# Kernel optimization log

Hardware: AMD Instinct MI355X
Metric: run time of the kernel (lower is better)

The kernel has to match this reference:

```python
import jax, jax.numpy as jnp
import numpy as np

D_MODEL = 1024
N_HEAD = 16
D_K = D_MODEL // N_HEAD
B, S = 4, 2048


def setup_inputs() -> dict:
    key = jax.random.key(0)
    ks = jax.random.split(key, 12)
    def w(k):
        return jax.random.normal(k, (D_MODEL, D_MODEL), dtype=jnp.float32) * 0.02
    def b(k):
        return jax.random.normal(k, (D_MODEL,), dtype=jnp.float32) * 0.02
    return {
        "x": jax.random.normal(ks[0], (B, S, D_MODEL), dtype=jnp.float32),
        "pos_emb": jax.random.normal(ks[1], (S, D_MODEL), dtype=jnp.float32),
        "Wq": w(ks[2]), "bq": b(ks[3]),
        "Wk": w(ks[4]), "bk": b(ks[5]),
        "Wv": w(ks[6]), "bv": b(ks[7]),
        "Wp": w(ks[8]), "bp": b(ks[9]),
        "Wo": w(ks[10]), "bo": b(ks[11]),
    }


def reference(x, pos_emb, Wq, bq, Wk, bk, Wv, bv, Wp, bp, Wo, bo):
    # x: [B, S, D]; pos_emb: [S, D]. cache=None path (prefill): kv_len == S.
    Bsz, Sl, _ = x.shape
    def heads(t):  # [B, S, D] -> [B, H, S, dk]
        return t.reshape(Bsz, Sl, N_HEAD, D_K).transpose(0, 2, 1, 3)
    q = heads(x @ Wq.T + bq)
    k = heads(x @ Wk.T + bk)
    v = heads(x @ Wv.T + bv)
    # pos projection: [S, D] -> [H, S, dk]
    p = (pos_emb @ Wp.T + bp).reshape(Sl, N_HEAD, D_K).transpose(1, 0, 2)
    q_pos = q + p[None]  # broadcast over batch
    scores = jnp.einsum("bhqd,bhkd->bhqk", q_pos, k) / jnp.sqrt(jnp.asarray(D_K, x.dtype))
    # causal mask: triu(ones(S, S), diagonal=1) positions are masked
    causal = jnp.tril(jnp.ones((Sl, Sl), dtype=bool))  # True = keep
    scores = jnp.where(causal[None, None], scores, -jnp.inf)
    attn = jax.nn.softmax(scores, axis=-1)  # dropout is identity (eval / p=0)
    out = jnp.einsum("bhqk,bhkd->bhqd", attn, v)
    out = out.transpose(0, 2, 1, 3).reshape(Bsz, Sl, D_MODEL)
    return out @ Wo.T + bo
```

## Files before the change

### kernel.cpp

```cpp
#include <hip/hip_runtime.h>

#define D_MODEL 1024
#define N_HEADS 16
#define DK 64
#define BATCH 4
#define SEQ 2048
#define MROWS (BATCH * SEQ)
#define TILE_E (256 * 64)

typedef float f32x4 __attribute__((ext_vector_type(4)));
typedef short bf16x8 __attribute__((ext_vector_type(8)));
typedef unsigned short u16;
typedef unsigned short u16x8 __attribute__((ext_vector_type(8)));

__device__ __forceinline__ float bf2f(u16 u) {
    union { unsigned int i; float f; } v; v.i = ((unsigned int)u) << 16; return v.f;
}
__device__ __forceinline__ u16 f2bf(float f) {
    union { float f; unsigned int i; } v; v.f = f;
    unsigned int u = v.i;
    u += 0x7fffu + ((u >> 16) & 1u);
    return (u16)(u >> 16);
}
__device__ __forceinline__ unsigned int pk2(float a, float b) {
    union { float f; unsigned int i; } ua, ub; ua.f = a; ub.f = b;
    return __builtin_amdgcn_perm(ub.i + 0x8000u, ua.i + 0x8000u, 0x07060302u);
}
__device__ __forceinline__ unsigned int cvtpk(float a, float b) {
    unsigned int r;
    asm("v_cvt_pk_bf16_f32 %0, %1, %2" : "=v"(r) : "v"(a), "v"(b));
    return r;
}

typedef unsigned int u32_as1 __attribute__((address_space(1)));
typedef unsigned int u32_as3 __attribute__((address_space(3)));
__device__ __forceinline__ void gload16(const u16* g, u16* l) {
    __builtin_amdgcn_global_load_lds((const u32_as1*)g, (u32_as3*)l, 16, 0, 0);
}

__global__ __launch_bounds__(256) void convert_all(
    const float* __restrict__ x, const float* __restrict__ pe,
    const float* __restrict__ w0, const float* __restrict__ w1, const float* __restrict__ w2,
    const float* __restrict__ w3, const float* __restrict__ w4,
    u16* __restrict__ xb, u16* __restrict__ pb,
    u16* __restrict__ wb0, u16* __restrict__ wb1, u16* __restrict__ wb2,
    u16* __restrict__ wb3, u16* __restrict__ wb4)
{
    int t = blockIdx.x * 256 + threadIdx.x;
    const float* src; u16* dst; int idx;
    if (t < 1048576)      { src = x;  dst = xb; idx = t; }
    else if (t < 1310720) { src = pe; dst = pb; idx = t - 1048576; }
    else {
        int r = t - 1310720; int w = r >> 17; idx = r & 131071;
        if      (w == 0) { src = w0; dst = wb0; }
        else if (w == 1) { src = w1; dst = wb1; }
        else if (w == 2) { src = w2; dst = wb2; }
        else if (w == 3) { src = w3; dst = wb3; }
        else             { src = w4; dst = wb4; }
    }
    const float4* p = (const float4*)src + (size_t)idx * 2;
    float4 a = p[0], b = p[1];
    u16x8 o;
    o[0] = f2bf(a.x); o[1] = f2bf(a.y); o[2] = f2bf(a.z); o[3] = f2bf(a.w);
    o[4] = f2bf(b.x); o[5] = f2bf(b.y); o[6] = f2bf(b.z); o[7] = f2bf(b.w);
    *((u16x8*)dst + idx) = o;
}

#define SA(bufp, h, kk) do { \
    gload16(Ag + (size_t)((h) * 64) * 1024 + (kk),       (bufp) + ((h) * 64 + wv * 8) * 64); \
    gload16(Ag + (size_t)((h) * 64 + 128) * 1024 + (kk), (bufp) + ((h) * 64 + 128 + wv * 8) * 64); \
} while (0)
#define SB(bufp, h, kk) do { \
    gload16(Wg + (size_t)((h) * 32) * 1024 + (kk),       (bufp) + (wq2 * 64 + (h) * 32 + w3 * 8) * 64); \
    gload16(Wg + (size_t)((h) * 32 + 128) * 1024 + (kk), (bufp) + (128 + wq2 * 64 + (h) * 32 + w3 * 8) * 64); \
} while (0)
#define LOAD_A(mh) \
    _Pragma("unroll") \
    for (int mi = 0; mi < 4; ++mi) { \
        aA[mi][0] = *(const bf16x8*)&Abuf[aoff0 + ((mh) * 64 + mi * 16) * 64]; \
        aA[mi][1] = *(const bf16x8*)&Abuf[aoff1 + ((mh) * 64 + mi * 16) * 64]; \
    }
#define LOAD_B(nh) \
    _Pragma("unroll") \
    for (int ni = 0; ni < 2; ++ni) { \
        bB[nh][ni][0] = *(const bf16x8*)&Bbuf[boff0 + ((nh) * 32 + ni * 16) * 64]; \
        bB[nh][ni][1] = *(const bf16x8*)&Bbuf[boff1 + ((nh) * 32 + ni * 16) * 64]; \
    }
#define MFMA16(mh, nh) \
    _Pragma("unroll") \
    for (int ks = 0; ks < 2; ++ks) \
        _Pragma("unroll") \
        for (int mi = 0; mi < 4; ++mi) \
            _Pragma("unroll") \
            for (int ni = 0; ni < 2; ++ni) \
                acc[(mh) * 4 + mi][(nh) * 2 + ni] = __builtin_amdgcn_mfma_f32_16x16x32_bf16( \
                    aA[mi][ks], bB[nh][ni][ks], acc[(mh) * 4 + mi][(nh) * 2 + ni], 0, 0, 0);

__device__ __forceinline__ void gemm256_loop(
    const u16* __restrict__ Ag, const u16* __restrict__ Wg,
    u16* AsBase, u16* BsBase, int wv,
    int aoff0, int aoff1, int boff0, int boff1, f32x4 (&acc)[8][4])
{
    const int wq2 = wv >> 2, w3 = wv & 3;
    bf16x8 aA[4][2], bB[2][2][2];

    SA(AsBase, 0, 0); SB(BsBase, 0, 0); SB(BsBase, 1, 0); SA(AsBase, 1, 0);
    SA(AsBase + TILE_E, 0, 64); SB(BsBase + TILE_E, 0, 64); SA(AsBase + TILE_E, 1, 64);
    asm volatile("s_waitcnt vmcnt(6)" ::: "memory");
    __builtin_amdgcn_s_barrier();

    for (int T = 0; T < 16; ++T) {
        u16* Abuf = AsBase + (T & 1) * TILE_E;
        u16* Bbuf = BsBase + (T & 1) * TILE_E;
        u16* Both = BsBase + ((T & 1) ^ 1) * TILE_E;
        const int k2 = T * 64 + 128;

        LOAD_A(0); LOAD_B(0);
        if (T < 15) SB(Both, 1, T * 64 + 64);
        __builtin_amdgcn_s_barrier();
        asm volatile("s_waitcnt lgkmcnt(0)" ::: "memory");
        __builtin_amdgcn_s_setprio(1); MFMA16(0, 0); __builtin_amdgcn_s_setprio(0);
        __builtin_amdgcn_s_barrier();

        LOAD_B(1);
        if (T < 14) SA(Abuf, 0, k2);
        __builtin_amdgcn_s_barrier();
        asm volatile("s_waitcnt lgkmcnt(0)" ::: "memory");
        __builtin_amdgcn_s_setprio(1); MFMA16(0, 1); __builtin_amdgcn_s_setprio(0);
        __builtin_amdgcn_s_barrier();

        LOAD_A(1);
        if (T < 14) SB(Bbuf, 0, k2);
        __builtin_amdgcn_s_barrier();
        asm volatile("s_waitcnt lgkmcnt(0)" ::: "memory");
        __builtin_amdgcn_s_setprio(1); MFMA16(1, 0); __builtin_amdgcn_s_setprio(0);
        __builtin_amdgcn_s_barrier();

        if (T < 14) SA(Abuf, 1, k2);
        __builtin_amdgcn_s_barrier();
        __builtin_amdgcn_s_setprio(1); MFMA16(1, 1); __builtin_amdgcn_s_setprio(0);
        if (T < 14)      { asm volatile("s_waitcnt vmcnt(6)" ::: "memory"); }
        else if (T < 15) { asm volatile("s_waitcnt vmcnt(0)" ::: "memory"); }
        __builtin_amdgcn_s_barrier();
    }
}

__global__ __launch_bounds__(512, 2) void qkv_gemm256(
    const u16* __restrict__ xb, const u16* __restrict__ peb,
    const u16* __restrict__ wqb, const u16* __restrict__ wkb,
    const u16* __restrict__ wvb, const u16* __restrict__ wpb,
    const float* __restrict__ bq, const float* __restrict__ bk,
    const float* __restrict__ bv, const float* __restrict__ bp,
    u16* __restrict__ Qb, u16* __restrict__ Kb, u16* __restrict__ V3,
    u16* __restrict__ Pb)
{
    __shared__ __align__(16) u16 SH[4 * TILE_E];
    u16* As = SH;
    u16* Bs = SH + 2 * TILE_E;

    const int tid  = threadIdx.x;
    const int lane = tid & 63;
    const int wv   = tid >> 6;
    const int l15  = lane & 15;
    const int quad = lane >> 4;
    const int wm = wv >> 2, wn = wv & 3;

    int wg = (blockIdx.x & 7) * 52 + (blockIdx.x >> 3);
    int chunk, m0, n0;
    if (wg < 384) {
        int g = wg >> 5;
        chunk = g >> 2; n0 = (g & 3) * 256; m0 = (wg & 31) * 256;
    } else {
        int r = wg - 384;
        chunk = 3; n0 = (r >> 3) * 256; m0 = (r & 7) * 256;
    }

    const u16* Abase = (chunk == 3) ? peb : xb;
    const u16* Wbase = (chunk == 0) ? wqb : ((chunk == 1) ? wkb : ((chunk == 2) ? wvb : wpb));

    const int trow = tid >> 3;
    const int swz  = ((tid & 7) ^ (trow & 7)) * 8;
    const u16* Ag = Abase + (size_t)(m0 + trow) * 1024 + swz;
    const u16* Wg = Wbase + (size_t)(n0 + (wv >> 2) * 64 + (trow & 31)) * 1024 + swz;

    const int x7 = l15 & 7;
    const int aoff0 = (wm * 128 + l15) * 64 + ((quad    ) ^ x7) * 8;
    const int aoff1 = (wm * 128 + l15) * 64 + ((quad + 4) ^ x7) * 8;
    const int boff0 = (wn * 64 + l15) * 64 + ((quad    ) ^ x7) * 8;
    const int boff1 = (wn * 64 + l15) * 64 + ((quad + 4) ^ x7) * 8;

    f32x4 acc[8][4];
#pragma unroll
    for (int i = 0; i < 8; ++i)
#pragma unroll
        for (int j = 0; j < 4; ++j) acc[i][j] = f32x4{0.f, 0.f, 0.f, 0.f};

    gemm256_loop(Ag, Wg, As, Bs, wv, aoff0, aoff1, boff0, boff1, acc);

    const float* bias = (chunk == 0) ? bq : ((chunk == 1) ? bk : ((chunk == 2) ? bv : bp));
    const int r0 = quad * 4;
    if (chunk == 2) {
#pragma unroll
        for (int n = 0; n < 4; ++n) {
            int col = n0 + wn * 64 + n * 16 + l15;
            float bvv = bias[col];
#pragma unroll
            for (int m = 0; m < 8; ++m) {
                int row0 = m0 + wm * 128 + m * 16 + r0;
                int hh = col >> 6, d = col & 63;
                int bb = row0 >> 11, sl = row0 & 2047;
                union { u16 h[4]; uint2 v; } pk;
#pragma unroll
                for (int r = 0; r < 4; ++r) pk.h[r] = f2bf(acc[m][n][r] + bvv);
                *((uint2*)V3 + ((size_t)(bb * 16 + hh) * 512 + (sl >> 2)) * 64 + d) = pk.v;
            }
        }
    } else {
        u16* dst = (chunk == 0) ? Qb : ((chunk == 1) ? Kb : Pb);
#pragma unroll
        for (int p = 0; p < 2; ++p) {
            __syncthreads();
            if (wm == p) {
#pragma unroll
                for (int n = 0; n < 4; ++n) {
                    int colL = wn * 64 + n * 16 + l15;
                    float bvv = bias[n0 + colL];
#pragma unroll
                    for (int m = 0; m < 8; ++m) {
#pragma unroll
                        for (int r = 0; r < 4; ++r)
                            SH[(m * 16 + r0 + r) * 264 + colL] = f2bf(acc[m][n][r] + bvv);
                    }
                }
            }
            __syncthreads();
            const int rbase = m0 + p * 128;
#pragma unroll
            for (int s = 0; s < 2; ++s) {
                int rowL = (tid >> 3) + s * 64;
#pragma unroll
                for (int i = 0; i < 4; ++i) {
                    int cc = (tid & 7) + i * 8;
                    *(u16x8*)(dst + (size_t)(rbase + rowL) * 1024 + n0 + cc * 8) =
                        *(const u16x8*)&SH[rowL * 264 + cc * 8];
                }
            }
        }
    }
}

#undef SA
#undef SB
#undef LOAD_A
#undef LOAD_B
#undef MFMA16

#define A_TILE (256 * 64)
#define B_TILE (128 * 64)
#define SAo(bufp, h, kk) do { \
    gload16(Ag + (size_t)((h) * 32) * 1024 + (kk),     (bufp) + (adst + (h) * 32) * 64); \
    gload16(Ag + (size_t)((h) * 32 + 8) * 1024 + (kk), (bufp) + (adst + (h) * 32 + 8) * 64); \
} while (0)
#define SBo(bufp, nh, kk) \
    gload16(Wg + (size_t)((nh) * 32) * 1024 + (kk), (bufp) + (bdst + (nh) * 32) * 64)
#define LAo(mh) \
    _Pragma("unroll") \
    for (int mi = 0; mi < 2; ++mi) { \
        aA[mi][0] = *(const bf16x8*)&Abuf[aoff0 + ((mh) * 32 + mi * 16) * 64]; \
        aA[mi][1] = *(const bf16x8*)&Abuf[aoff1 + ((mh) * 32 + mi * 16) * 64]; \
    }
#define LBo(nh) \
    _Pragma("unroll") \
    for (int ni = 0; ni < 2; ++ni) { \
        bB[nh][ni][0] = *(const bf16x8*)&Bbuf[boff0 + ((nh) * 32 + ni * 16) * 64]; \
        bB[nh][ni][1] = *(const bf16x8*)&Bbuf[boff1 + ((nh) * 32 + ni * 16) * 64]; \
    }
#define MMo(mh, nh) \
    _Pragma("unroll") \
    for (int ks = 0; ks < 2; ++ks) \
        _Pragma("unroll") \
        for (int mi = 0; mi < 2; ++mi) \
            _Pragma("unroll") \
            for (int ni = 0; ni < 2; ++ni) \
                acc[(mh) * 2 + mi][(nh) * 2 + ni] = __builtin_amdgcn_mfma_f32_16x16x32_bf16( \
                    aA[mi][ks], bB[nh][ni][ks], acc[(mh) * 2 + mi][(nh) * 2 + ni], 0, 0, 0);

__global__ __launch_bounds__(512, 2) void gemm_out256n(
    const u16* __restrict__ A, const u16* __restrict__ W,
    const float* __restrict__ bias, float* __restrict__ Cout)
{
    __shared__ __align__(16) u16 As[2 * A_TILE];
    __shared__ __align__(16) u16 Bs[2 * B_TILE];

    const int tid  = threadIdx.x;
    const int lane = tid & 63;
    const int wv   = tid >> 6;
    const int l15  = lane & 15;
    const int quad = lane >> 4;
    const int wm = wv >> 1, wn = wv & 1;

    int wg = (blockIdx.x & 7) * 32 + (blockIdx.x >> 3);
    const int m0 = (wg >> 3) * 256;
    const int n0 = (wg & 7) * 128;

    const int swz    = ((tid & 7) ^ ((tid >> 3) & 7)) * 8;
    const int arow_t = (wv >> 1) * 64 + (wv & 1) * 16 + (lane >> 3);
    const int brow_t = (wv >> 2) * 64 + (wv & 3) * 8 + (lane >> 3);
    const u16* Ag = A + (size_t)(m0 + arow_t) * 1024 + swz;
    const u16* Wg = W + (size_t)(n0 + brow_t) * 1024 + swz;
    const int adst = (wv >> 1) * 64 + (wv & 1) * 16;
    const int bdst = (wv >> 2) * 64 + (wv & 3) * 8;

    const int x7 = l15 & 7;
    const int aoff0 = (wm * 64 + l15) * 64 + ((quad    ) ^ x7) * 8;
    const int aoff1 = (wm * 64 + l15) * 64 + ((quad + 4) ^ x7) * 8;
    const int boff0 = (wn * 64 + l15) * 64 + ((quad    ) ^ x7) * 8;
    const int boff1 = (wn * 64 + l15) * 64 + ((quad + 4) ^ x7) * 8;

    f32x4 acc[4][4];
#pragma unroll
    for (int i = 0; i < 4; ++i)
#pragma unroll
        for (int j = 0; j < 4; ++j) acc[i][j] = f32x4{0.f, 0.f, 0.f, 0.f};
    bf16x8 aA[2][2], bB[2][2][2];

    SAo(As, 0, 0); SBo(Bs, 0, 0); SBo(Bs, 1, 0); SAo(As, 1, 0);
    SAo(As + A_TILE, 0, 64); SBo(Bs + B_TILE, 0, 64); SAo(As + A_TILE, 1, 64);
    asm volatile("s_waitcnt vmcnt(5)" ::: "memory");
    __builtin_amdgcn_s_barrier();

    for (int T = 0; T < 16; ++T) {
        u16* Abuf = As + (T & 1) * A_TILE;
        u16* Bbuf = Bs + (T & 1) * B_TILE;
        u16* Both = Bs + ((T & 1) ^ 1) * B_TILE;
        const int k2 = T * 64 + 128;

        LAo(0); LBo(0);
        if (T < 15) SBo(Both, 1, T * 64 + 64);
        __builtin_amdgcn_s_barrier();
        asm volatile("s_waitcnt lgkmcnt(0)" ::: "memory");
        __builtin_amdgcn_s_setprio(1); MMo(0, 0); __builtin_amdgcn_s_setprio(0);
        __builtin_amdgcn_s_barrier();

        LBo(1);
        if (T < 14) SAo(Abuf, 0, k2);
        __builtin_amdgcn_s_barrier();
        asm volatile("s_waitcnt lgkmcnt(0)" ::: "memory");
        __builtin_amdgcn_s_setprio(1); MMo(0, 1); __builtin_amdgcn_s_setprio(0);
        __builtin_amdgcn_s_barrier();

        LAo(1);
        if (T < 14) SBo(Bbuf, 0, k2);
        __builtin_amdgcn_s_barrier();
        asm volatile("s_waitcnt lgkmcnt(0)" ::: "memory");
        __builtin_amdgcn_s_setprio(1); MMo(1, 0); __builtin_amdgcn_s_setprio(0);
        __builtin_amdgcn_s_barrier();

        if (T < 14) SAo(Abuf, 1, k2);
        __builtin_amdgcn_s_barrier();
        __builtin_amdgcn_s_setprio(1); MMo(1, 1); __builtin_amdgcn_s_setprio(0);
        if (T < 14)      { asm volatile("s_waitcnt vmcnt(5)" ::: "memory"); }
        else if (T < 15) { asm volatile("s_waitcnt vmcnt(0)" ::: "memory"); }
        __builtin_amdgcn_s_barrier();
    }

    const int r0 = quad * 4;
#pragma unroll
    for (int b2 = 0; b2 < 4; ++b2) {
        int col = n0 + wn * 64 + (b2 >> 1) * 32 + (b2 & 1) * 16 + l15;
        float bvv = bias[col];
#pragma unroll
        for (int a = 0; a < 4; ++a) {
            int row0 = m0 + wm * 64 + (a >> 1) * 32 + (a & 1) * 16 + r0;
#pragma unroll
            for (int r = 0; r < 4; ++r)
                Cout[(size_t)(row0 + r) * 1024 + col] = acc[a][b2][r] + bvv;
        }
    }
}
#undef SAo
#undef SBo
#undef LAo
#undef LBo
#undef MMo

__global__ __launch_bounds__(256, 4) void flash_attn_mfma(
    const u16* __restrict__ Q, const u16* __restrict__ Kq,
    const u16* __restrict__ V3, const u16* __restrict__ Pb, u16* __restrict__ O)
{
    __shared__ __align__(16) u16 Ks[2][64 * 72];
    __shared__ __align__(16) u16 Vs[2][64 * 72];

    const int tid  = threadIdx.x;
    const int lane = tid & 63;
    const int wv   = tid >> 6;
    const int l15  = lane & 15;
    const int quad = lane >> 4;
    const int gg   = blockIdx.x;
    const int h    = gg & 15;
    const int b    = gg >> 4;
    const int y    = 15 - (int)blockIdx.y;
    const int wq0  = y * 128 + wv * 32;
    const int NT   = 2 * y + 2;

    bf16x8 qf[2][2];
    const size_t qrowbase = (size_t)(b * SEQ) * D_MODEL + h * DK;
#pragma unroll
    for (int qb = 0; qb < 2; ++qb)
#pragma unroll
        for (int ks = 0; ks < 2; ++ks) {
            int qrow = wq0 + qb * 16 + l15;
            u16x8 qr = *(const u16x8*)(Q + qrowbase + (size_t)qrow * D_MODEL + ks * 32 + quad * 8);
            u16x8 pr = *(const u16x8*)(Pb + (size_t)qrow * D_MODEL + h * DK + ks * 32 + quad * 8);
            u16x8 o;
#pragma unroll
            for (int t = 0; t < 8; ++t)
                o[t] = f2bf((bf2f(qr[t]) + bf2f(pr[t])) * 0.180336880111120f);
            qf[qb][ks] = *(bf16x8*)&o;
        }

    f32x4 Oacc[2][4];
#pragma unroll
    for (int i = 0; i < 2; ++i)
#pragma unroll
        for (int jj = 0; jj < 4; ++jj) Oacc[i][jj] = f32x4{0.f, 0.f, 0.f, 0.f};
    float l_r[2] = {0.f, 0.f};

    const int sr  = tid >> 2;
    const int sc8 = (tid & 3) * 16;
    const u16* Kg = Kq + (size_t)(b * SEQ + sr) * D_MODEL + h * DK + sc8;

    const uint2* Vgp = (const uint2*)V3 + (size_t)gg * 32768 + tid;
    const int vd = tid & 63;
    int vb[4];
#pragma unroll
    for (int i = 0; i < 4; ++i) {
        int g16 = (tid >> 6) + 4 * i;
        vb[i] = (g16 >> 3) * 32 + (g16 & 3) * 8 + ((g16 >> 2) & 1) * 4;
    }

    u16x8 kr0 = *(const u16x8*)Kg;
    u16x8 kr1 = *(const u16x8*)(Kg + 8);
    uint2 vr0 = Vgp[0], vr1 = Vgp[256], vr2 = Vgp[512], vr3 = Vgp[768];

    *(u16x8*)&Ks[0][sr * 72 + sc8]     = kr0;
    *(u16x8*)&Ks[0][sr * 72 + sc8 + 8] = kr1;
    *(uint2*)&Vs[0][vd * 72 + vb[0]] = vr0;
    *(uint2*)&Vs[0][vd * 72 + vb[1]] = vr1;
    *(uint2*)&Vs[0][vd * 72 + vb[2]] = vr2;
    *(uint2*)&Vs[0][vd * 72 + vb[3]] = vr3;
    __syncthreads();

    for (int kt = 0; kt < NT; ++kt) {
        const int cur = kt & 1;
        if (kt + 1 < NT) {
            const u16* Kn = Kg + (size_t)(kt + 1) * 64 * D_MODEL;
            kr0 = *(const u16x8*)Kn;
            kr1 = *(const u16x8*)(Kn + 8);
            vr0 = Vgp[(size_t)(kt + 1) * 1024];
            vr1 = Vgp[(size_t)(kt + 1) * 1024 + 256];
            vr2 = Vgp[(size_t)(kt + 1) * 1024 + 512];
            vr3 = Vgp[(size_t)(kt + 1) * 1024 + 768];
        }

        if (kt * 64 <= wq0 + 31) {
            f32x4 sacc[4][2];
#pragma unroll
            for (int kb = 0; kb < 4; ++kb)
#pragma unroll
                for (int qb = 0; qb < 2; ++qb) sacc[kb][qb] = f32x4{0.f, 0.f, 0.f, 0.f};
            __builtin_amdgcn_s_setprio(1);
#pragma unroll
            for (int ks = 0; ks < 2; ++ks) {
                bf16x8 kf[4];
#pragma unroll
                for (int kb = 0; kb < 4; ++kb)
                    kf[kb] = *(const bf16x8*)&Ks[cur][(kb * 16 + l15) * 72 + ks * 32 + quad * 8];
#pragma unroll
                for (int kb = 0; kb < 4; ++kb)
#pragma unroll
                    for (int qb = 0; qb < 2; ++qb)
                        sacc[kb][qb] = __builtin_amdgcn_mfma_f32_16x16x32_bf16(kf[kb], qf[qb][ks], sacc[kb][qb], 0, 0, 0);
            }
            __builtin_amdgcn_s_setprio(0);

            if (kt * 64 + 63 > wq0) {
#pragma unroll
                for (int kb = 0; kb < 4; ++kb) {
                    int key_g = kt * 64 + kb * 16 + quad * 4;
#pragma unroll
                    for (int qb = 0; qb < 2; ++qb) {
                        int q_g = wq0 + qb * 16 + l15;
#pragma unroll
                        for (int r = 0; r < 4; ++r)
                            if (key_g + r > q_g) sacc[kb][qb][r] = -1e30f;
                    }
                }
            }

            bf16x8 pf[2][2];
#pragma unroll
            for (int qb = 0; qb < 2; ++qb) {
                float s = 0.f;
                float p[4][4];
#pragma unroll
                for (int kb = 0; kb < 4; ++kb) {
                    p[kb][0] = __builtin_amdgcn_exp2f(sacc[kb][qb][0]);
                    p[kb][1] = __builtin_amdgcn_exp2f(sacc[kb][qb][1]);
                    p[kb][2] = __builtin_amdgcn_exp2f(sacc[kb][qb][2]);
                    p[kb][3] = __builtin_amdgcn_exp2f(sacc[kb][qb][3]);
                    s += (p[kb][0] + p[kb][1]) + (p[kb][2] + p[kb][3]);
                }
                l_r[qb] += s;
#pragma unroll
                for (int ks = 0; ks < 2; ++ks) {
                    union { unsigned int w[4]; bf16x8 v; } u;
                    u.w[0] = cvtpk(p[2 * ks][0],     p[2 * ks][1]);
                    u.w[1] = cvtpk(p[2 * ks][2],     p[2 * ks][3]);
                    u.w[2] = cvtpk(p[2 * ks + 1][0], p[2 * ks + 1][1]);
                    u.w[3] = cvtpk(p[2 * ks + 1][2], p[2 * ks + 1][3]);
                    pf[qb][ks] = u.v;
                }
            }

            __builtin_amdgcn_s_setprio(1);
#pragma unroll
            for (int ks = 0; ks < 2; ++ks) {
                bf16x8 vf[4];
#pragma unroll
                for (int db = 0; db < 4; ++db)
                    vf[db] = *(const bf16x8*)&Vs[cur][(db * 16 + l15) * 72 + ks * 32 + quad * 8];
#pragma unroll
                for (int qb = 0; qb < 2; ++qb)
#pragma unroll
                    for (int db = 0; db < 4; ++db)
                        Oacc[qb][db] = __builtin_amdgcn_mfma_f32_16x16x32_bf16(pf[qb][ks], vf[db], Oacc[qb][db], 0, 0, 0);
            }
            __builtin_amdgcn_s_setprio(0);
        }

        if (kt + 1 < NT) {
            *(u16x8*)&Ks[cur ^ 1][sr * 72 + sc8]     = kr0;
            *(u16x8*)&Ks[cur ^ 1][sr * 72 + sc8 + 8] = kr1;
            *(uint2*)&Vs[cur ^ 1][vd * 72 + vb[0]] = vr0;
            *(uint2*)&Vs[cur ^ 1][vd * 72 + vb[1]] = vr1;
            *(uint2*)&Vs[cur ^ 1][vd * 72 + vb[2]] = vr2;
            *(uint2*)&Vs[cur ^ 1][vd * 72 + vb[3]] = vr3;
        }
        __syncthreads();
    }

    float linv[2];
#pragma unroll
    for (int qb = 0; qb < 2; ++qb) {
        float s = l_r[qb];
        s += __shfl_xor(s, 16);
        s += __shfl_xor(s, 32);
        linv[qb] = 1.f / s;
    }
#pragma unroll
    for (int qb = 0; qb < 2; ++qb)
#pragma unroll
        for (int r = 0; r < 4; ++r) {
            float li = __shfl(linv[qb], quad * 4 + r);
            size_t row = (size_t)(b * SEQ + wq0 + qb * 16 + quad * 4 + r) * D_MODEL + h * DK;
#pragma unroll
            for (int db = 0; db < 4; ++db)
                O[row + db * 16 + l15] = f2bf(Oacc[qb][db][r] * li);
        }
}

extern "C" void kernel_launch(void* const* d_in, const int* in_sizes, int n_in,
                              void* d_out, int out_size, void* d_ws, size_t ws_size,
                              hipStream_t stream) {
    const float* x  = (const float*)d_in[0];
    const float* pe = (const float*)d_in[1];
    const float* Wq = (const float*)d_in[2];  const float* bq = (const float*)d_in[3];
    const float* Wk = (const float*)d_in[4];  const float* bk = (const float*)d_in[5];
    const float* Wv = (const float*)d_in[6];  const float* bv = (const float*)d_in[7];
    const float* Wp = (const float*)d_in[8];  const float* bp = (const float*)d_in[9];
    const float* Wo = (const float*)d_in[10]; const float* bo = (const float*)d_in[11];
    float* out = (float*)d_out;
    char* ws = (char*)d_ws;

    size_t off = 0;
    u16* xb  = (u16*)(ws + off); off += (size_t)MROWS * D_MODEL * 2;
    u16* peb = (u16*)(ws + off); off += (size_t)SEQ * D_MODEL * 2;
    u16* wqb = (u16*)(ws + off); off += (size_t)D_MODEL * D_MODEL * 2;
    u16* wkb = (u16*)(ws + off); off += (size_t)D_MODEL * D_MODEL * 2;
    u16* wvb = (u16*)(ws + off); off += (size_t)D_MODEL * D_MODEL * 2;
    u16* wpb = (u16*)(ws + off); off += (size_t)D_MODEL * D_MODEL * 2;
    u16* wob = (u16*)(ws + off); off += (size_t)D_MODEL * D_MODEL * 2;
    u16* Qb  = (u16*)(ws + off); off += (size_t)MROWS * D_MODEL * 2;
    u16* Kb  = (u16*)(ws + off); off += (size_t)MROWS * D_MODEL * 2;
    u16* V3b = (u16*)(ws + off); off += (size_t)MROWS * D_MODEL * 2;
    u16* Pb  = (u16*)(ws + off); off += (size_t)SEQ * D_MODEL * 2;
    u16* AO = xb;

    convert_all<<<7680, 256, 0, stream>>>(x, pe, Wq, Wk, Wv, Wp, Wo,
                                          xb, peb, wqb, wkb, wvb, wpb, wob);

    qkv_gemm256<<<416, 512, 0, stream>>>(
        xb, peb, wqb, wkb, wvb, wpb, bq, bk, bv, bp, Qb, Kb, V3b, Pb);

    flash_attn_mfma<<<dim3(64, 16), 256, 0, stream>>>(Qb, Kb, V3b, Pb, AO);

    gemm_out256n<<<256, 512, 0, stream>>>(AO, wob, bo, out);
}
```

Before: 257.7 us.

## Use two waves per attention block with 64 query rows each and interleaved tile order

The flash attention kernel moves from four waves of 32 query rows to two waves of 64 query rows per 128-row block. Each K/V tile read from shared memory now feeds twice as many MFMAs, and each thread loads twice as much of the next tile. The query-tile ordering across blockIdx.y is also changed to interleave long and short causal tiles. The cost is more accumulator registers per wave and fewer waves per block, which may reduce latency hiding, and causal skipping now happens at 64-row granularity, so more tiles are partly masked.

Result: slower. 268.4 us (+4.1%).

```diff
diff --git a/kernel.cpp b/kernel.cpp
--- a/kernel.cpp
+++ b/kernel.cpp
@@ -384,7 +384,7 @@
 #undef LBo
 #undef MMo
 
-__global__ __launch_bounds__(256, 4) void flash_attn_mfma(
+__global__ __launch_bounds__(128, 2) void flash_attn_mfma(
     const u16* __restrict__ Q, const u16* __restrict__ Kq,
     const u16* __restrict__ V3, const u16* __restrict__ Pb, u16* __restrict__ O)
 {
@@ -399,14 +399,16 @@
     const int gg   = blockIdx.x;
     const int h    = gg & 15;
     const int b    = gg >> 4;
-    const int y    = 15 - (int)blockIdx.y;
-    const int wq0  = y * 128 + wv * 32;
+    const int by   = blockIdx.y;
+    const int y    = (by < 4) ? (15 - by) : (by < 8) ? (by + 4)
+                   : (by < 12) ? (15 - by) : (by - 12);
+    const int wq0  = y * 128 + wv * 64;
     const int NT   = 2 * y + 2;
 
-    bf16x8 qf[2][2];
+    bf16x8 qf[4][2];
     const size_t qrowbase = (size_t)(b * SEQ) * D_MODEL + h * DK;
 #pragma unroll
-    for (int qb = 0; qb < 2; ++qb)
+    for (int qb = 0; qb < 4; ++qb)
 #pragma unroll
         for (int ks = 0; ks < 2; ++ks) {
             int qrow = wq0 + qb * 16 + l15;
@@ -419,56 +421,53 @@
             qf[qb][ks] = *(bf16x8*)&o;
         }
 
-    f32x4 Oacc[2][4];
-#pragma unroll
-    for (int i = 0; i < 2; ++i)
+    f32x4 Oacc[4][4];
+#pragma unroll
+    for (int i = 0; i < 4; ++i)
 #pragma unroll
         for (int jj = 0; jj < 4; ++jj) Oacc[i][jj] = f32x4{0.f, 0.f, 0.f, 0.f};
-    float l_r[2] = {0.f, 0.f};
-
-    const int sr  = tid >> 2;
-    const int sc8 = (tid & 3) * 16;
-    const u16* Kg = Kq + (size_t)(b * SEQ + sr) * D_MODEL + h * DK + sc8;
-
+    float l_r[4] = {0.f, 0.f, 0.f, 0.f};
+
+    const u16* Kg = Kq + (size_t)(b * SEQ + (tid >> 3)) * D_MODEL + h * DK + (tid & 7) * 8;
+    const int krow = (tid >> 3);
+    const int kcol = (tid & 7) * 8;
     const uint2* Vgp = (const uint2*)V3 + (size_t)gg * 32768 + tid;
     const int vd = tid & 63;
-    int vb[4];
-#pragma unroll
-    for (int i = 0; i < 4; ++i) {
-        int g16 = (tid >> 6) + 4 * i;
+    int vb[8];
+#pragma unroll
+    for (int i = 0; i < 8; ++i) {
+        int g16 = (tid >> 6) + 2 * i;
         vb[i] = (g16 >> 3) * 32 + (g16 & 3) * 8 + ((g16 >> 2) & 1) * 4;
     }
 
-    u16x8 kr0 = *(const u16x8*)Kg;
-    u16x8 kr1 = *(const u16x8*)(Kg + 8);
-    uint2 vr0 = Vgp[0], vr1 = Vgp[256], vr2 = Vgp[512], vr3 = Vgp[768];
-
-    *(u16x8*)&Ks[0][sr * 72 + sc8]     = kr0;
-    *(u16x8*)&Ks[0][sr * 72 + sc8 + 8] = kr1;
-    *(uint2*)&Vs[0][vd * 72 + vb[0]] = vr0;
-    *(uint2*)&Vs[0][vd * 72 + vb[1]] = vr1;
-    *(uint2*)&Vs[0][vd * 72 + vb[2]] = vr2;
-    *(uint2*)&Vs[0][vd * 72 + vb[3]] = vr3;
+    u16x8 kr[4]; uint2 vr[8];
+#pragma unroll
+    for (int i = 0; i < 4; ++i) kr[i] = *(const u16x8*)(Kg + (size_t)i * 16 * D_MODEL);
+#pragma unroll
+    for (int i = 0; i < 8; ++i) vr[i] = Vgp[128 * i];
+
+#pragma unroll
+    for (int i = 0; i < 4; ++i) *(u16x8*)&Ks[0][(krow + 16 * i) * 72 + kcol] = kr[i];
+#pragma unroll
+    for (int i = 0; i < 8; ++i) *(uint2*)&Vs[0][vd * 72 + vb[i]] = vr[i];
     __syncthreads();
 
     for (int kt = 0; kt < NT; ++kt) {
         const int cur = kt & 1;
         if (kt + 1 < NT) {
             const u16* Kn = Kg + (size_t)(kt + 1) * 64 * D_MODEL;
-            kr0 = *(const u16x8*)Kn;
-            kr1 = *(const u16x8*)(Kn + 8);
-            vr0 = Vgp[(size_t)(kt + 1) * 1024];
-            vr1 = Vgp[(size_t)(kt + 1) * 1024 + 256];
-            vr2 = Vgp[(size_t)(kt + 1) * 1024 + 512];
-            vr3 = Vgp[(size_t)(kt + 1) * 1024 + 768];
-        }
-
-        if (kt * 64 <= wq0 + 31) {
-            f32x4 sacc[4][2];
+#pragma unroll
+            for (int i = 0; i < 4; ++i) kr[i] = *(const u16x8*)(Kn + (size_t)i * 16 * D_MODEL);
+#pragma unroll
+            for (int i = 0; i < 8; ++i) vr[i] = Vgp[(size_t)(kt + 1) * 1024 + 128 * i];
+        }
+
+        if (kt * 64 <= wq0 + 63) {
+            f32x4 sacc[4][4];
 #pragma unroll
             for (int kb = 0; kb < 4; ++kb)
 #pragma unroll
-                for (int qb = 0; qb < 2; ++qb) sacc[kb][qb] = f32x4{0.f, 0.f, 0.f, 0.f};
+                for (int qb = 0; qb < 4; ++qb) sacc[kb][qb] = f32x4{0.f, 0.f, 0.f, 0.f};
             __builtin_amdgcn_s_setprio(1);
 #pragma unroll
             for (int ks = 0; ks < 2; ++ks) {
@@ -479,7 +478,7 @@
 #pragma unroll
                 for (int kb = 0; kb < 4; ++kb)
 #pragma unroll
-                    for (int qb = 0; qb < 2; ++qb)
+                    for (int qb = 0; qb < 4; ++qb)
                         sacc[kb][qb] = __builtin_amdgcn_mfma_f32_16x16x32_bf16(kf[kb], qf[qb][ks], sacc[kb][qb], 0, 0, 0);
             }
             __builtin_amdgcn_s_setprio(0);
@@ -489,7 +488,7 @@
                 for (int kb = 0; kb < 4; ++kb) {
                     int key_g = kt * 64 + kb * 16 + quad * 4;
 #pragma unroll
-                    for (int qb = 0; qb < 2; ++qb) {
+                    for (int qb = 0; qb < 4; ++qb) {
                         int q_g = wq0 + qb * 16 + l15;
 #pragma unroll
                         for (int r = 0; r < 4; ++r)
@@ -498,9 +497,9 @@
                 }
             }
 
-            bf16x8 pf[2][2];
-#pragma unroll
-            for (int qb = 0; qb < 2; ++qb) {
+            bf16x8 pf[4][2];
+#pragma unroll
+            for (int qb = 0; qb < 4; ++qb) {
                 float s = 0.f;
                 float p[4][4];
 #pragma unroll
@@ -531,7 +530,7 @@
                 for (int db = 0; db < 4; ++db)
                     vf[db] = *(const bf16x8*)&Vs[cur][(db * 16 + l15) * 72 + ks * 32 + quad * 8];
 #pragma unroll
-                for (int qb = 0; qb < 2; ++qb)
+                for (int qb = 0; qb < 4; ++qb)
 #pragma unroll
                     for (int db = 0; db < 4; ++db)
                         Oacc[qb][db] = __builtin_amdgcn_mfma_f32_16x16x32_bf16(pf[qb][ks], vf[db], Oacc[qb][db], 0, 0, 0);
@@ -540,26 +539,24 @@
         }
 
         if (kt + 1 < NT) {
-            *(u16x8*)&Ks[cur ^ 1][sr * 72 + sc8]     = kr0;
-            *(u16x8*)&Ks[cur ^ 1][sr * 72 + sc8 + 8] = kr1;
-            *(uint2*)&Vs[cur ^ 1][vd * 72 + vb[0]] = vr0;
-            *(uint2*)&Vs[cur ^ 1][vd * 72 + vb[1]] = vr1;
-            *(uint2*)&Vs[cur ^ 1][vd * 72 + vb[2]] = vr2;
-            *(uint2*)&Vs[cur ^ 1][vd * 72 + vb[3]] = vr3;
+#pragma unroll
+            for (int i = 0; i < 4; ++i) *(u16x8*)&Ks[cur ^ 1][(krow + 16 * i) * 72 + kcol] = kr[i];
+#pragma unroll
+            for (int i = 0; i < 8; ++i) *(uint2*)&Vs[cur ^ 1][vd * 72 + vb[i]] = vr[i];
         }
         __syncthreads();
     }
 
-    float linv[2];
-#pragma unroll
-    for (int qb = 0; qb < 2; ++qb) {
+    float linv[4];
+#pragma unroll
+    for (int qb = 0; qb < 4; ++qb) {
         float s = l_r[qb];
         s += __shfl_xor(s, 16);
         s += __shfl_xor(s, 32);
         linv[qb] = 1.f / s;
     }
 #pragma unroll
-    for (int qb = 0; qb < 2; ++qb)
+    for (int qb = 0; qb < 4; ++qb)
 #pragma unroll
         for (int r = 0; r < 4; ++r) {
             float li = __shfl(linv[qb], quad * 4 + r);
@@ -603,7 +600,7 @@
     qkv_gemm256<<<416, 512, 0, stream>>>(
         xb, peb, wqb, wkb, wvb, wpb, bq, bk, bv, bp, Qb, Kb, V3b, Pb);
 
-    flash_attn_mfma<<<dim3(64, 16), 256, 0, stream>>>(Qb, Kb, V3b, Pb, AO);
+    flash_attn_mfma<<<dim3(64, 16), 128, 0, stream>>>(Qb, Kb, V3b, Pb, AO);
 
     gemm_out256n<<<256, 512, 0, stream>>>(AO, wob, bo, out);
 }
```
